# Performance work log

Hardware: AMD Instinct MI355X
Metric: run time of the kernel (lower is better)

## Reference

```python
import jax, jax.numpy as jnp
import numpy as np
import itertools

N_BITS = 64   # data_info['n']
K_MAX = 3     # data_info['k']
BATCH = 8192


def _build_table(n, k):
    # All 0/1 vectors of length n with at most k ones, ordered by popcount then lexicographic
    rows = [np.zeros((1, n), dtype=np.int32)]
    for i in range(1, k + 1):
        idxs = np.array(list(itertools.combinations(range(n), i)), dtype=np.int64)  # (C(n,i), i)
        t = np.zeros((idxs.shape[0], n), dtype=np.int32)
        t[np.arange(idxs.shape[0])[:, None], idxs] = 1
        rows.append(t)
    return np.concatenate(rows, axis=0)  # (total_case, n)


def setup_inputs() -> dict:
    key = jax.random.key(0)
    table_np = _build_table(N_BITS, K_MAX)
    total_case = table_np.shape[0]  # 43745 for n=64, k=3
    k1, k2 = jax.random.split(key)
    # x must exactly match a table row (original code's .nonzero()[0] assumes a match exists)
    sel = jax.random.randint(k1, (BATCH,), 0, total_case)
    table = jnp.asarray(table_np)
    x = table[sel]  # (BATCH, n) int32, each row has <= k ones
    W = jax.random.normal(k2, (total_case,), dtype=jnp.float32)
    return {"x": x, "table": table, "W": W}


def reference(x, table, W):
    # Original per-sample loop: idx_i = first row r with sum(table[r] ^ x_i) == 0.
    # For 0/1 vectors, sum(a ^ b) = sum(a) + sum(b) - 2 * (a . b), so the whole
    # batch reduces to one GEMM + an equality test + argmax (first True).
    xf = x.astype(jnp.float32)
    tf = table.astype(jnp.float32)
    xs = jnp.sum(xf, axis=1)          # (B,)
    ts = jnp.sum(tf, axis=1)          # (T,)
    dot = xf @ tf.T                   # (B, T)
    mismatch = xs[:, None] + ts[None, :] - 2.0 * dot  # (B, T) popcount of XOR
    idx = jnp.argmax(mismatch == 0.0, axis=1)         # first exact match per row
    logw = jnp.log(jax.nn.softmax(W))                 # matches torch: log(softmax(W))
    return logw[idx]                                  # (B,)
```

## Files before the change

kernel.cpp:

```cpp
#include <hip/hip_runtime.h>

__global__ __launch_bounds__(256) void fused_rank_kernel(
        const int* __restrict__ x,
        const float* __restrict__ W, int T,
        float* __restrict__ out, int batch) {
    __shared__ float red[4];
    __shared__ float s_lse;
    const int tid  = threadIdx.x;
    const int lane = tid & 63;
    const int wave = tid >> 6;

    const int wave_row0 = blockIdx.x * 64 + wave * 16;
    int vals[16];
    #pragma unroll
    for (int r = 0; r < 16; ++r) {
        const int row = wave_row0 + r;
        vals[r] = (row < batch) ? x[(size_t)row * 64 + lane] : 0;
    }

    float s = 0.0f;
    const int T4 = T >> 2;
    const float4* __restrict__ W4 = (const float4*)W;
    for (int i = tid; i < T4; i += 256) {
        const float4 v = W4[i];
        s += __expf(v.x) + __expf(v.y) + __expf(v.z) + __expf(v.w);
    }
    for (int i = (T4 << 2) + tid; i < T; i += 256)
        s += __expf(W[i]);
    #pragma unroll
    for (int off = 32; off > 0; off >>= 1) s += __shfl_down(s, off, 64);
    if (lane == 0) red[wave] = s;
    __syncthreads();
    if (tid == 0) s_lse = __logf(red[0] + red[1] + red[2] + red[3]);
    __syncthreads();
    const float lse = s_lse;

    unsigned long long mymask = 0ull;
    #pragma unroll
    for (int r = 0; r < 16; ++r) {
        const unsigned long long mk = __ballot(vals[r] != 0);
        if (lane == r) mymask = mk;
    }

    if (lane < 16) {
        const int row = wave_row0 + lane;
        if (row < batch) {
            const int m = __popcll(mymask);
            int idx;
            if (m == 0) {
                idx = 0;
            } else {
                unsigned long long t = mymask;
                const int a = __builtin_ctzll(t); t &= t - 1;
                if (m == 1) {
                    idx = 1 + a;
                } else {
                    const int b = __builtin_ctzll(t); t &= t - 1;
                    if (m == 2) {
                        idx = 65 + ((4032 - (63 - a) * (64 - a)) >> 1) + (b - a - 1);
                    } else {
                        const int c = __builtin_ctzll(t);
                        const int s1 = 41664 - ((64 - a) * (63 - a) * (62 - a)) / 6;
                        const int s2 = ((62 - a) * (63 - a) - (63 - b) * (64 - b)) >> 1;
                        idx = 2081 + s1 + s2 + (c - b - 1);
                    }
                }
            }
            out[row] = W[idx] - lse;
        }
    }
}

extern "C" void kernel_launch(void* const* d_in, const int* in_sizes, int n_in,
                              void* d_out, int out_size, void* d_ws, size_t ws_size,
                              hipStream_t stream) {
    const int*   x = (const int*)d_in[0];
    const float* W = (const float*)d_in[2];
    float* out     = (float*)d_out;
    (void)d_ws; (void)ws_size;

    const int T = in_sizes[2];
    const int B = in_sizes[0] / 64;

    const int blocks = (B + 63) / 64;
    fused_rank_kernel<<<blocks, 256, 0, stream>>>(x, W, T, out, B);
}
```

Baseline: 79.87 us.

## Split softmax normalizer across blocks with cooperative grid sync

Previously every block recomputed the full sum of exp(W) over all table entries. Now each block sums a disjoint slice into a workspace partial, a cooperative grid sync follows, and each block reduces the partials to get the log-sum-exp. Rows per block are halved so more blocks share the work. This adds a cooperative launch and a grid-wide barrier, and it requires all blocks to be co-resident.

```diff
diff --git a/kernel.cpp b/kernel.cpp
--- a/kernel.cpp
+++ b/kernel.cpp
@@ -1,19 +1,25 @@
 #include <hip/hip_runtime.h>
+#include <hip/hip_cooperative_groups.h>
 
-__global__ __launch_bounds__(256) void fused_rank_kernel(
+namespace cg = cooperative_groups;
+
+__global__ __launch_bounds__(256) void fused_coop_kernel(
         const int* __restrict__ x,
         const float* __restrict__ W, int T,
-        float* __restrict__ out, int batch) {
+        float* __restrict__ out, int batch,
+        float* __restrict__ partials) {
     __shared__ float red[4];
     __shared__ float s_lse;
     const int tid  = threadIdx.x;
     const int lane = tid & 63;
     const int wave = tid >> 6;
+    const int bid  = blockIdx.x;
+    const int nb   = gridDim.x;
 
-    const int wave_row0 = blockIdx.x * 64 + wave * 16;
-    int vals[16];
+    const int wave_row0 = bid * 32 + wave * 8;
+    int vals[8];
     #pragma unroll
-    for (int r = 0; r < 16; ++r) {
+    for (int r = 0; r < 8; ++r) {
         const int row = wave_row0 + r;
         vals[r] = (row < batch) ? x[(size_t)row * 64 + lane] : 0;
     }
@@ -21,28 +27,38 @@
     float s = 0.0f;
     const int T4 = T >> 2;
     const float4* __restrict__ W4 = (const float4*)W;
-    for (int i = tid; i < T4; i += 256) {
+    for (int i = bid * 256 + tid; i < T4; i += 256 * nb) {
         const float4 v = W4[i];
         s += __expf(v.x) + __expf(v.y) + __expf(v.z) + __expf(v.w);
     }
-    for (int i = (T4 << 2) + tid; i < T; i += 256)
+    for (int i = (T4 << 2) + bid * 256 + tid; i < T; i += 256 * nb)
         s += __expf(W[i]);
     #pragma unroll
     for (int off = 32; off > 0; off >>= 1) s += __shfl_down(s, off, 64);
     if (lane == 0) red[wave] = s;
     __syncthreads();
-    if (tid == 0) s_lse = __logf(red[0] + red[1] + red[2] + red[3]);
+    if (tid == 0) partials[bid] = red[0] + red[1] + red[2] + red[3];
+
+    cg::this_grid().sync();
+
+    if (wave == 0) {
+        float p = 0.0f;
+        for (int i = lane; i < nb; i += 64) p += partials[i];
+        #pragma unroll
+        for (int off = 32; off > 0; off >>= 1) p += __shfl_down(p, off, 64);
+        if (lane == 0) s_lse = __logf(p);
+    }
     __syncthreads();
     const float lse = s_lse;
 
     unsigned long long mymask = 0ull;
     #pragma unroll
-    for (int r = 0; r < 16; ++r) {
+    for (int r = 0; r < 8; ++r) {
         const unsigned long long mk = __ballot(vals[r] != 0);
         if (lane == r) mymask = mk;
     }
 
-    if (lane < 16) {
+    if (lane < 8) {
         const int row = wave_row0 + lane;
         if (row < batch) {
             const int m = __popcll(mymask);
@@ -76,12 +92,15 @@
                               hipStream_t stream) {
     const int*   x = (const int*)d_in[0];
     const float* W = (const float*)d_in[2];
-    float* out     = (float*)d_out;
-    (void)d_ws; (void)ws_size;
+    float* out      = (float*)d_out;
+    float* partials = (float*)d_ws;
 
     const int T = in_sizes[2];
     const int B = in_sizes[0] / 64;
 
-    const int blocks = (B + 63) / 64;
-    fused_rank_kernel<<<blocks, 256, 0, stream>>>(x, W, T, out, B);
+    const int blocks = (B + 31) / 32;
+    void* args[] = { (void*)&x, (void*)&W, (void*)&T,
+                     (void*)&out, (void*)&B, (void*)&partials };
+    hipLaunchCooperativeKernel((const void*)fused_coop_kernel,
+                               dim3(blocks), dim3(256), args, 0, stream);
 }
```

After: 106.8 us. +33.7%, slower.

## Split softmax denominator across blocks with atomic grid barrier

Applied to the files above, without the earlier changes.

Previously every block recomputed the full sum of exp(W) over all table entries. Now each of a fixed 128 blocks sums only a strided slice, publishes its partial to workspace, and bumps an atomic counter. All blocks spin-wait until the counter reaches the block count, then each block re-reduces the partials to get the log-sum-exp. This removes redundant exp work and W reads, at the cost of an extra memset launch and a grid-wide spin barrier that requires all blocks to be co-resident. The fixed grid of 128 blocks only covers batches up to 8192 rows.

```diff
diff --git a/kernel.cpp b/kernel.cpp
--- a/kernel.cpp
+++ b/kernel.cpp
@@ -1,16 +1,19 @@
 #include <hip/hip_runtime.h>
 
-__global__ __launch_bounds__(256) void fused_rank_kernel(
+__global__ __launch_bounds__(256) void fused_kernel(
         const int* __restrict__ x,
         const float* __restrict__ W, int T,
-        float* __restrict__ out, int batch) {
+        float* __restrict__ out, int batch,
+        int* __restrict__ counter,
+        float* __restrict__ partials, int nblocks) {
     __shared__ float red[4];
     __shared__ float s_lse;
     const int tid  = threadIdx.x;
     const int lane = tid & 63;
     const int wave = tid >> 6;
+    const int bid  = blockIdx.x;
 
-    const int wave_row0 = blockIdx.x * 64 + wave * 16;
+    const int wave_row0 = bid * 64 + wave * 16;
     int vals[16];
     #pragma unroll
     for (int r = 0; r < 16; ++r) {
@@ -21,19 +24,23 @@
     float s = 0.0f;
     const int T4 = T >> 2;
     const float4* __restrict__ W4 = (const float4*)W;
-    for (int i = tid; i < T4; i += 256) {
+    for (int i = bid * 256 + tid; i < T4; i += nblocks * 256) {
         const float4 v = W4[i];
         s += __expf(v.x) + __expf(v.y) + __expf(v.z) + __expf(v.w);
     }
-    for (int i = (T4 << 2) + tid; i < T; i += 256)
+    for (int i = (T4 << 2) + bid * 256 + tid; i < T; i += nblocks * 256)
         s += __expf(W[i]);
     #pragma unroll
     for (int off = 32; off > 0; off >>= 1) s += __shfl_down(s, off, 64);
     if (lane == 0) red[wave] = s;
     __syncthreads();
-    if (tid == 0) s_lse = __logf(red[0] + red[1] + red[2] + red[3]);
-    __syncthreads();
-    const float lse = s_lse;
+    if (tid == 0) {
+        const float p = red[0] + red[1] + red[2] + red[3];
+        __hip_atomic_store(&partials[bid], p,
+                           __ATOMIC_RELAXED, __HIP_MEMORY_SCOPE_AGENT);
+        __hip_atomic_fetch_add(counter, 1,
+                               __ATOMIC_RELEASE, __HIP_MEMORY_SCOPE_AGENT);
+    }
 
     unsigned long long mymask = 0ull;
     #pragma unroll
@@ -41,34 +48,52 @@
         const unsigned long long mk = __ballot(vals[r] != 0);
         if (lane == r) mymask = mk;
     }
-
-    if (lane < 16) {
-        const int row = wave_row0 + lane;
-        if (row < batch) {
-            const int m = __popcll(mymask);
-            int idx;
-            if (m == 0) {
-                idx = 0;
+    const int myrow  = wave_row0 + lane;
+    const bool active = (lane < 16) && (myrow < batch);
+    float wv = 0.0f;
+    if (active) {
+        const int m = __popcll(mymask);
+        int idx;
+        if (m == 0) {
+            idx = 0;
+        } else {
+            unsigned long long t = mymask;
+            const int a = __builtin_ctzll(t); t &= t - 1;
+            if (m == 1) {
+                idx = 1 + a;
             } else {
-                unsigned long long t = mymask;
-                const int a = __builtin_ctzll(t); t &= t - 1;
-                if (m == 1) {
-                    idx = 1 + a;
+                const int b = __builtin_ctzll(t); t &= t - 1;
+                if (m == 2) {
+                    idx = 65 + ((4032 - (63 - a) * (64 - a)) >> 1) + (b - a - 1);
                 } else {
-                    const int b = __builtin_ctzll(t); t &= t - 1;
-                    if (m == 2) {
-                        idx = 65 + ((4032 - (63 - a) * (64 - a)) >> 1) + (b - a - 1);
-                    } else {
-                        const int c = __builtin_ctzll(t);
-                        const int s1 = 41664 - ((64 - a) * (63 - a) * (62 - a)) / 6;
-                        const int s2 = ((62 - a) * (63 - a) - (63 - b) * (64 - b)) >> 1;
-                        idx = 2081 + s1 + s2 + (c - b - 1);
-                    }
+                    const int c = __builtin_ctzll(t);
+                    const int s1 = 41664 - ((64 - a) * (63 - a) * (62 - a)) / 6;
+                    const int s2 = ((62 - a) * (63 - a) - (63 - b) * (64 - b)) >> 1;
+                    idx = 2081 + s1 + s2 + (c - b - 1);
                 }
             }
-            out[row] = W[idx] - lse;
         }
+        wv = W[idx];
     }
+
+    if (tid == 0) {
+        while (__hip_atomic_load(counter, __ATOMIC_ACQUIRE,
+                                 __HIP_MEMORY_SCOPE_AGENT) < nblocks)
+            __builtin_amdgcn_s_sleep(1);
+    }
+    __syncthreads();
+
+    if (wave == 0) {
+        float p = 0.0f;
+        for (int i = lane; i < nblocks; i += 64)
+            p += __hip_atomic_load(&partials[i], __ATOMIC_RELAXED,
+                                   __HIP_MEMORY_SCOPE_AGENT);
+        #pragma unroll
+        for (int off = 32; off > 0; off >>= 1) p += __shfl_down(p, off, 64);
+        if (lane == 0) s_lse = __logf(p);
+    }
+    __syncthreads();
+    if (active) out[myrow] = wv - s_lse;
 }
 
 extern "C" void kernel_launch(void* const* d_in, const int* in_sizes, int n_in,
@@ -76,12 +101,16 @@
                               hipStream_t stream) {
     const int*   x = (const int*)d_in[0];
     const float* W = (const float*)d_in[2];
-    float* out     = (float*)d_out;
-    (void)d_ws; (void)ws_size;
+    float* out = (float*)d_out;
+
+    int*   counter  = (int*)d_ws;
+    float* partials = (float*)((char*)d_ws + 256);
 
     const int T = in_sizes[2];
     const int B = in_sizes[0] / 64;
 
-    const int blocks = (B + 63) / 64;
-    fused_rank_kernel<<<blocks, 256, 0, stream>>>(x, W, T, out, B);
+    const int nblocks = 128;
+    hipMemsetAsync(counter, 0, sizeof(int), stream);
+    fused_kernel<<<nblocks, 256, 0, stream>>>(x, W, T, out, B,
+                                              counter, partials, nblocks);
 }
```

Result: faster. 78.14 us (-2.2%).
